# Optimization experiments

Hardware: AMD Instinct MI355X
Metric: run time of the kernel (lower is better)

The kernel has to match this reference:

```python
import jax, jax.numpy as jnp
import numpy as np

N = 100000      # nodes
E = 1600000     # edges
IN = 128        # in_channels
HID = 32        # hidden_channels
HEADS = 4
G = 256         # number of graphs in the batch
NEG_SLOPE = 0.2


def setup_inputs() -> dict:
    key = jax.random.key(0)
    ks = jax.random.split(key, 20)
    s = 0.1
    d = {
        'x': jax.random.normal(ks[0], (N, IN), jnp.float32),
        'edge_index': jax.random.randint(ks[1], (2, E), 0, N, dtype=jnp.int64),
        'batch': jnp.sort(jax.random.randint(ks[2], (N,), 0, G, dtype=jnp.int64)),
        # conv1: IN -> HID per head, HEADS heads, concat
        'W1': jax.random.normal(ks[3], (IN, HEADS * HID), jnp.float32) * s,
        'a_src1': jax.random.normal(ks[4], (HEADS, HID), jnp.float32) * s,
        'a_dst1': jax.random.normal(ks[5], (HEADS, HID), jnp.float32) * s,
        'b1': jnp.zeros((HEADS * HID,), jnp.float32),
        # conv2: HEADS*HID -> HID per head, HEADS heads, concat
        'W2': jax.random.normal(ks[6], (HEADS * HID, HEADS * HID), jnp.float32) * s,
        'a_src2': jax.random.normal(ks[7], (HEADS, HID), jnp.float32) * s,
        'a_dst2': jax.random.normal(ks[8], (HEADS, HID), jnp.float32) * s,
        'b2': jnp.zeros((HEADS * HID,), jnp.float32),
        # conv3: HEADS*HID -> HID, 1 head, no concat (mean over heads is identity)
        'W3': jax.random.normal(ks[9], (HEADS * HID, HID), jnp.float32) * s,
        'a_src3': jax.random.normal(ks[10], (1, HID), jnp.float32) * s,
        'a_dst3': jax.random.normal(ks[11], (1, HID), jnp.float32) * s,
        'b3': jnp.zeros((HID,), jnp.float32),
        # final readout
        'fc_w': jax.random.normal(ks[12], (HID, 1), jnp.float32) * s,
        'fc_b': jnp.zeros((1,), jnp.float32),
    }
    return d


def _gat_layer(x, src, dst, W, a_s, a_d, b, concat):
    """One PyG-style GATConv: edge attention logits, per-destination softmax, scatter-aggregate."""
    n = x.shape[0]
    H, C = a_s.shape
    h = (x @ W).reshape(n, H, C)                       # [N, H, C]
    asrc = (h * a_s).sum(-1)                           # [N, H]
    adst = (h * a_d).sum(-1)                           # [N, H]
    e = jax.nn.leaky_relu(asrc[src] + adst[dst], NEG_SLOPE)   # [Etot, H]
    m = jax.ops.segment_max(e, dst, num_segments=n)    # per-dst max (self-loops guarantee non-empty)
    ex = jnp.exp(e - m[dst])
    den = jax.ops.segment_sum(ex, dst, num_segments=n)
    alpha = ex / (den[dst] + 1e-16)                    # segment softmax, [Etot, H]
    out = jax.ops.segment_sum(alpha[:, :, None] * h[src], dst, num_segments=n)  # [N, H, C]
    if concat:
        return out.reshape(n, H * C) + b
    return out.mean(axis=1) + b


def reference(x, edge_index, batch, W1, a_src1, a_dst1, b1, W2, a_src2, a_dst2, b2,
              W3, a_src3, a_dst3, b3, fc_w, fc_b):
    n = x.shape[0]
    loops = jnp.arange(n, dtype=edge_index.dtype)      # GATConv adds self-loops by default
    src = jnp.concatenate([edge_index[0], loops])
    dst = jnp.concatenate([edge_index[1], loops])

    h = jax.nn.elu(_gat_layer(x, src, dst, W1, a_src1, a_dst1, b1, True))
    h = jax.nn.elu(_gat_layer(h, src, dst, W2, a_src2, a_dst2, b2, True))
    h = jax.nn.elu(_gat_layer(h, src, dst, W3, a_src3, a_dst3, b3, False))

    counts = jax.ops.segment_sum(jnp.ones((n,), h.dtype), batch, num_segments=G)
    pooled = jax.ops.segment_sum(h, batch, num_segments=G) / jnp.maximum(counts, 1.0)[:, None]
    # dropout p=0.5 is identity in eval mode
    return pooled @ fc_w + fc_b                        # [G, 1]
```

## Files before the change

kernel.cpp:

```cpp
#include <hip/hip_runtime.h>
#include <hip/hip_bf16.h>
#include <math.h>

#define NEG_SLOPE 0.2f
#define CHUNK 6144

typedef short bf16x8 __attribute__((ext_vector_type(8)));
typedef float f32x4  __attribute__((ext_vector_type(4)));

__device__ __forceinline__ float leaky(float x){ return x > 0.f ? x : NEG_SLOPE*x; }
__device__ __forceinline__ float elu(float x){ return x > 0.f ? x : expm1f(x); }

__device__ __forceinline__ ushort f2bf(float f){
  uint u = __float_as_uint(f);
  u += 0x7fffu + ((u >> 16) & 1u);
  return (ushort)(u >> 16);
}
__device__ __forceinline__ uint pk2(float lo, float hi){
  return (uint)f2bf(lo) | ((uint)f2bf(hi) << 16);
}
__device__ __forceinline__ float2 bfpair(uint v){
  return make_float2(__uint_as_float(v << 16), __uint_as_float(v & 0xffff0000u));
}

__global__ __launch_bounds__(256) void k_histA(const int* __restrict__ ei, int E,
                                               int* __restrict__ bucketCount){
  __shared__ int hist[512];
  for (int b = threadIdx.x; b < 512; b += 256) hist[b] = 0;
  __syncthreads();
  int base = blockIdx.x * 2048;
  int cnt = min(2048, E - base);
  for (int i = threadIdx.x; i < cnt; i += 256)
    atomicAdd(&hist[ei[E + base + i] >> 8], 1);
  __syncthreads();
  for (int b = threadIdx.x; b < 512; b += 256)
    if (hist[b]) atomicAdd(&bucketCount[b], hist[b]);
}

__global__ __launch_bounds__(256) void k_scanB(const int* __restrict__ bucketCount, int NB,
                        int* __restrict__ bucketBase, int* __restrict__ gcursor, int E){
  __shared__ int s[512];
  for (int b = threadIdx.x; b < 512; b += 256)
    s[b] = (b < NB) ? bucketCount[b] : 0;
  __syncthreads();
  if (threadIdx.x == 0){
    int run = 0;
    for (int b = 0; b < NB; b++){ int v = s[b]; s[b] = run; run += v; }
  }
  __syncthreads();
  for (int b = threadIdx.x; b < NB; b += 256){
    bucketBase[b] = s[b]; gcursor[b] = s[b];
  }
  if (threadIdx.x == 0) bucketBase[NB] = E;
}

__global__ __launch_bounds__(256) void k_scatA(const int* __restrict__ ei, int E, int NB,
                         int* __restrict__ gcursor, uint* __restrict__ tmp){
  __shared__ uint stageS[CHUNK];
  __shared__ uint stageD[CHUNK];
  __shared__ int hist[512], pre[512], cur[512], gbase[512];
  __shared__ int scanArr[256];
  int tid = threadIdx.x;
  int base = blockIdx.x * CHUNK;
  int cnt = min(CHUNK, E - base);
  for (int b = tid; b < 512; b += 256) hist[b] = 0;
  __syncthreads();
  for (int i = tid; i < cnt; i += 256)
    atomicAdd(&hist[ei[E + base + i] >> 8], 1);
  __syncthreads();
  int a0 = hist[2*tid], a1 = hist[2*tid+1];
  scanArr[tid] = a0 + a1;
  __syncthreads();
  for (int st = 1; st < 256; st <<= 1){
    int v = (tid >= st) ? scanArr[tid - st] : 0;
    __syncthreads();
    scanArr[tid] += v;
    __syncthreads();
  }
  int eb = tid ? scanArr[tid-1] : 0;
  pre[2*tid] = eb;        cur[2*tid] = eb;
  pre[2*tid+1] = eb + a0; cur[2*tid+1] = eb + a0;
  if (2*tid < NB && a0 > 0)   gbase[2*tid]   = atomicAdd(&gcursor[2*tid],   a0);
  if (2*tid+1 < NB && a1 > 0) gbase[2*tid+1] = atomicAdd(&gcursor[2*tid+1], a1);
  __syncthreads();
  for (int i = tid; i < cnt; i += 256){
    int s = ei[base + i];
    int d = ei[E + base + i];
    int lpos = atomicAdd(&cur[d >> 8], 1);
    stageS[lpos] = (uint)s; stageD[lpos] = (uint)d;
  }
  __syncthreads();
  for (int i = tid; i < cnt; i += 256){
    uint d = stageD[i];
    int b = d >> 8;
    tmp[gbase[b] + (i - pre[b])] = (stageS[i] << 8) | (d & 255u);
  }
}

__global__ __launch_bounds__(256) void k_csr(const uint* __restrict__ tmp,
                      const int* __restrict__ bucketBase,
                      int N, int NB, int* __restrict__ offsets, int* __restrict__ csr){
  int b = blockIdx.x;
  int nodeBase = b << 8;
  int nNodes = min(256, N - nodeBase);
  int eBeg = bucketBase[b], eEnd = bucketBase[b+1];
  __shared__ int deg[256], cur[256];
  int tid = threadIdx.x;
  deg[tid] = 0;
  __syncthreads();
  for (int e = eBeg + tid; e < eEnd; e += 256)
    atomicAdd(&deg[tmp[e] & 255u], 1);
  __syncthreads();
  cur[tid] = deg[tid];
  __syncthreads();
  for (int st = 1; st < 256; st <<= 1){
    int w = (tid >= st) ? cur[tid - st] : 0;
    __syncthreads();
    cur[tid] += w;
    __syncthreads();
  }
  int excl = tid ? cur[tid-1] : 0;
  __syncthreads();
  cur[tid] = excl;
  if (tid < nNodes) offsets[nodeBase + tid] = eBeg + excl;
  if (b == NB-1 && tid == 0) offsets[N] = eEnd;
  __syncthreads();
  for (int e = eBeg + tid; e < eEnd; e += 256){
    uint u = tmp[e];
    int lpos = atomicAdd(&cur[u & 255u], 1);
    csr[eBeg + lpos] = (int)(u >> 8);
  }
}

template<int NT>
__global__ __launch_bounds__(256) void k_wrep(const float* __restrict__ W, ushort* __restrict__ Wf){
  int idx = blockIdx.x*256 + threadIdx.x;
  if (idx >= NT*4*64) return;
  int lane = idx & 63;
  int c = (idx >> 6) & 3;
  int t = idx >> 8;
  int col = t*16 + (lane & 15);
  int k0 = c*32 + (lane >> 4)*8;
  uint4 o;
  const float* p0 = W + (size_t)k0*(NT*16) + col;
  o.x = pk2(p0[0],          p0[NT*16]);
  o.y = pk2(p0[2*NT*16],    p0[3*NT*16]);
  o.z = pk2(p0[4*NT*16],    p0[5*NT*16]);
  o.w = pk2(p0[6*NT*16],    p0[7*NT*16]);
  *(uint4*)(Wf + (size_t)idx*8) = o;
}

template<int NT, bool A_F32>
__global__ __launch_bounds__(256) void k_mgemm(const void* __restrict__ Xv,
                     const ushort* __restrict__ Wf, ushort* __restrict__ Y, int n){
  constexpr int M = NT*16;
  int lane = threadIdx.x & 63;
  int l15 = lane & 15, q = lane >> 4;
  int wgid = blockIdx.x*4 + (threadIdx.x >> 6);
  int nchunks = (n + 15) >> 4;
  int stride = gridDim.x*4;

  bf16x8 bw[NT][4];
  #pragma unroll
  for (int t = 0; t < NT; t++)
    #pragma unroll
    for (int c = 0; c < 4; c++)
      bw[t][c] = *(const bf16x8*)(Wf + (size_t)(((t<<2)+c)*64 + lane)*8);

  int chunk = wgid;
  if (chunk >= nchunks) return;

  bf16x8 aCur[4], aNext[4];
  auto loadA = [&](int ck, bf16x8* a){
    int m = ck*16 + l15;
    if (m >= n) m = n - 1;
    if (A_F32){
      const float* X = (const float*)Xv + (size_t)m*128 + q*8;
      #pragma unroll
      for (int c = 0; c < 4; c++){
        float4 u0 = *(const float4*)(X + c*32);
        float4 u1 = *(const float4*)(X + c*32 + 4);
        uint4 pkd;
        pkd.x = pk2(u0.x, u0.y); pkd.y = pk2(u0.z, u0.w);
        pkd.z = pk2(u1.x, u1.y); pkd.w = pk2(u1.z, u1.w);
        union { uint4 u; bf16x8 v; } cv; cv.u = pkd;
        a[c] = cv.v;
      }
    } else {
      const ushort* X = (const ushort*)Xv + (size_t)m*128 + q*8;
      #pragma unroll
      for (int c = 0; c < 4; c++) a[c] = *(const bf16x8*)(X + c*32);
    }
  };

  loadA(chunk, aCur);
  while (true){
    int nx = chunk + stride;
    if (nx < nchunks) loadA(nx, aNext);
    f32x4 acc[NT];
    #pragma unroll
    for (int t = 0; t < NT; t++) acc[t] = (f32x4){0.f,0.f,0.f,0.f};
    #pragma unroll
    for (int c = 0; c < 4; c++)
      #pragma unroll
      for (int t = 0; t < NT; t++)
        acc[t] = __builtin_amdgcn_mfma_f32_16x16x32_bf16(aCur[c], bw[t][c], acc[t], 0, 0, 0);
    int rowb = chunk*16 + q*4;
    #pragma unroll
    for (int t = 0; t < NT; t++)
      #pragma unroll
      for (int r = 0; r < 4; r++){
        int row = rowb + r;
        if (row < n) Y[(size_t)row*M + t*16 + l15] = f2bf(acc[t][r]);
      }
    if (nx >= nchunks) break;
    chunk = nx;
    #pragma unroll
    for (int c = 0; c < 4; c++) aCur[c] = aNext[c];
  }
}

__global__ __launch_bounds__(256) void k_attn(const ushort* __restrict__ Hb, const float* __restrict__ a_s,
                     const float* __restrict__ a_d, float* __restrict__ asrc, float* __restrict__ adst,
                     int n, int H, int M){
  int idx = blockIdx.x*256 + threadIdx.x;
  if (idx >= n*H) return;
  int node = idx / H, h = idx - node*H;
  const uint4* r4 = (const uint4*)(Hb + (size_t)node*M + h*32);
  const float* as = a_s + h*32;
  const float* ad = a_d + h*32;
  float s1 = 0.f, s2 = 0.f;
  #pragma unroll
  for (int i = 0; i < 4; i++){
    uint4 qv = r4[i];
    uint w[4] = {qv.x, qv.y, qv.z, qv.w};
    #pragma unroll
    for (int j = 0; j < 4; j++){
      float2 f = bfpair(w[j]);
      int c = i*8 + j*2;
      s1 += f.x*as[c] + f.y*as[c+1];
      s2 += f.x*ad[c] + f.y*ad[c+1];
    }
  }
  asrc[idx] = s1; adst[idx] = s2;
}

template<bool OUT_BF16>
__global__ __launch_bounds__(256) void k_agg128f(const ushort* __restrict__ Hb,
                    const float* __restrict__ asrc, const float* __restrict__ adst,
                    const int* __restrict__ offsets, const int* __restrict__ csr_src,
                    const float* __restrict__ bias, void* __restrict__ Out, int n){
  __shared__ float lwAll[4][256];
  __shared__ int   lsAll[4][64];
  int wv = threadIdx.x >> 6;
  int lane = threadIdx.x & 63;
  float* lw = lwAll[wv];
  int*   ls = lsAll[wv];
  int node = blockIdx.x*4 + wv;
  if (node >= n) return;
  const int up = lane, ch = up*2, h0 = up >> 4;
  const uint* rows = (const uint*)Hb;
  float4 adv = *(const float4*)(adst + (size_t)node*4);
  float adh = (h0==0)?adv.x:(h0==1)?adv.y:(h0==2)?adv.z:adv.w;
  float acc0 = 0.f, acc1 = 0.f, den = 0.f;
  {
    float w = __expf(leaky(asrc[(size_t)node*4 + h0] + adh));
    float2 f = bfpair(rows[(size_t)node*64 + up]);
    den += w; acc0 += w*f.x; acc1 += w*f.y;
  }
  int j0 = offsets[node], end = offsets[node+1];
  for (int base = j0; base < end; base += 64){
    int m = min(64, end - base);
    if (lane < m){
      int s = csr_src[base + lane];
      ls[lane] = s;
      float4 a = *(const float4*)(asrc + (size_t)s*4);
      float4 w4;
      w4.x = __expf(leaky(a.x + adv.x));
      w4.y = __expf(leaky(a.y + adv.y));
      w4.z = __expf(leaky(a.z + adv.z));
      w4.w = __expf(leaky(a.w + adv.w));
      *(float4*)(lw + lane*4) = w4;
    }
    int e = 0;
    for (; e + 8 <= m; e += 8){
      int s0=ls[e+0], s1=ls[e+1], s2=ls[e+2], s3=ls[e+3];
      int s4=ls[e+4], s5=ls[e+5], s6=ls[e+6], s7=ls[e+7];
      float w0=lw[(e+0)*4+h0], w1=lw[(e+1)*4+h0], w2=lw[(e+2)*4+h0], w3=lw[(e+3)*4+h0];
      float w4=lw[(e+4)*4+h0], w5=lw[(e+5)*4+h0], w6=lw[(e+6)*4+h0], w7=lw[(e+7)*4+h0];
      uint r0 = rows[(size_t)s0*64 + up];
      uint r1 = rows[(size_t)s1*64 + up];
      uint r2 = rows[(size_t)s2*64 + up];
      uint r3 = rows[(size_t)s3*64 + up];
      uint r4 = rows[(size_t)s4*64 + up];
      uint r5 = rows[(size_t)s5*64 + up];
      uint r6 = rows[(size_t)s6*64 + up];
      uint r7 = rows[(size_t)s7*64 + up];
      float2 f0=bfpair(r0), f1=bfpair(r1), f2=bfpair(r2), f3=bfpair(r3);
      float2 f4=bfpair(r4), f5=bfpair(r5), f6=bfpair(r6), f7=bfpair(r7);
      den  += ((w0+w1)+(w2+w3)) + ((w4+w5)+(w6+w7));
      acc0 += (w0*f0.x + w1*f1.x + w2*f2.x + w3*f3.x)
            + (w4*f4.x + w5*f5.x + w6*f6.x + w7*f7.x);
      acc1 += (w0*f0.y + w1*f1.y + w2*f2.y + w3*f3.y)
            + (w4*f4.y + w5*f5.y + w6*f6.y + w7*f7.y);
    }
    for (; e < m; e++){
      int s = ls[e];
      float w = lw[e*4 + h0];
      float2 f = bfpair(rows[(size_t)s*64 + up]);
      den += w; acc0 += w*f.x; acc1 += w*f.y;
    }
  }
  float inv = 1.f/(den + 1e-16f);
  float ox = elu(acc0*inv + bias[ch]);
  float oy = elu(acc1*inv + bias[ch+1]);
  if (OUT_BF16){
    ((uint*)Out)[(size_t)node*64 + up] = pk2(ox, oy);
  } else {
    *(float2*)((float*)Out + (size_t)node*128 + ch) = make_float2(ox, oy);
  }
}

__global__ __launch_bounds__(256) void k_agg32(const ushort* __restrict__ Hb,
                    const float* __restrict__ asrc, const float* __restrict__ adst,
                    const int* __restrict__ offsets, const int* __restrict__ csr_src,
                    const float* __restrict__ bias, float* __restrict__ Out, int n){
  __shared__ int   lsAll[4][4][16];
  __shared__ float lwAll[4][4][16];
  int wv = threadIdx.x >> 6;
  int lane = threadIdx.x & 63;
  int g = lane >> 4, i = lane & 15;
  int node = (blockIdx.x*4 + wv)*4 + g;
  if (node >= n) return;
  int* ls = lsAll[wv][g];
  float* lw = lwAll[wv][g];
  const uint* rows = (const uint*)Hb;
  float adn = adst[node];
  float acc0 = 0.f, acc1 = 0.f, den = 0.f;
  {
    float w = __expf(leaky(asrc[node] + adn));
    float2 f = bfpair(rows[(size_t)node*16 + i]);
    den += w; acc0 += w*f.x; acc1 += w*f.y;
  }
  int j0 = offsets[node], end = offsets[node+1];
  for (int base = j0; base < end; base += 16){
    int m = min(16, end - base);
    {
      int idx = base + i;
      bool v = idx < end;
      int s = v ? csr_src[idx] : node;
      ls[i] = s;
      lw[i] = v ? __expf(leaky(asrc[s] + adn)) : 0.f;
    }
    int mR = (m + 3) & ~3;
    for (int e = 0; e < mR; e += 4){
      int s0 = ls[e], s1 = ls[e+1], s2 = ls[e+2], s3 = ls[e+3];
      float w0 = lw[e], w1 = lw[e+1], w2 = lw[e+2], w3 = lw[e+3];
      uint r0 = rows[(size_t)s0*16 + i];
      uint r1 = rows[(size_t)s1*16 + i];
      uint r2 = rows[(size_t)s2*16 + i];
      uint r3 = rows[(size_t)s3*16 + i];
      float2 f0 = bfpair(r0), f1 = bfpair(r1), f2 = bfpair(r2), f3 = bfpair(r3);
      den  += (w0 + w1) + (w2 + w3);
      acc0 += w0*f0.x + w1*f1.x + w2*f2.x + w3*f3.x;
      acc1 += w0*f0.y + w1*f1.y + w2*f2.y + w3*f3.y;
    }
  }
  float inv = 1.f/(den + 1e-16f);
  int ch = i*2;
  float2 o;
  o.x = elu(acc0*inv + bias[ch]);
  o.y = elu(acc1*inv + bias[ch+1]);
  *(float2*)(Out + (size_t)node*32 + ch) = o;
}

__global__ __launch_bounds__(256) void k_bounds(const int* __restrict__ batch, int n, int G,
                                                int* __restrict__ gstart){
  int i = blockIdx.x*256 + threadIdx.x;
  if (i >= n) return;
  int b = batch[i];
  int bp = (i > 0) ? batch[i-1] : -1;
  for (int g = bp + 1; g <= b; g++) gstart[g] = i;
  if (i == n-1){
    for (int g = b + 1; g <= G; g++) gstart[g] = n;
  }
}

__global__ __launch_bounds__(256) void k_pool2(const float* __restrict__ H3,
                     const int* __restrict__ gstart, const float* __restrict__ fcw,
                     const float* __restrict__ fcb, float* __restrict__ out, int G){
  int g = blockIdx.x;
  int s0 = gstart[g], s1 = gstart[g+1];
  int tid = threadIdx.x;
  int c = tid & 31, r = tid >> 5;
  float sum = 0.f;
  for (int i = s0 + r; i < s1; i += 8)
    sum += H3[(size_t)i*32 + c];
  __shared__ float sh[8][32];
  sh[r][c] = sum;
  __syncthreads();
  if (tid < 32){
    float t = 0.f;
    #pragma unroll
    for (int k = 0; k < 8; k++) t += sh[k][tid];
    t *= fcw[tid];
    #pragma unroll
    for (int off = 16; off; off >>= 1) t += __shfl_down(t, off, 32);
    if (tid == 0){
      float cnt = (float)(s1 - s0); if (cnt < 1.f) cnt = 1.f;
      out[g] = t/cnt + fcb[0];
    }
  }
}

extern "C" void kernel_launch(void* const* d_in, const int* in_sizes, int n_in,
                              void* d_out, int out_size, void* d_ws, size_t ws_size,
                              hipStream_t stream){
  const float* x    = (const float*)d_in[0];
  const int*   ei   = (const int*)d_in[1];
  const int*   batch= (const int*)d_in[2];
  const float* W1   = (const float*)d_in[3];
  const float* as1  = (const float*)d_in[4];
  const float* ad1  = (const float*)d_in[5];
  const float* b1   = (const float*)d_in[6];
  const float* W2   = (const float*)d_in[7];
  const float* as2  = (const float*)d_in[8];
  const float* ad2  = (const float*)d_in[9];
  const float* b2   = (const float*)d_in[10];
  const float* W3   = (const float*)d_in[11];
  const float* as3  = (const float*)d_in[12];
  const float* ad3  = (const float*)d_in[13];
  const float* b3   = (const float*)d_in[14];
  const float* fcw  = (const float*)d_in[15];
  const float* fcb  = (const float*)d_in[16];
  float* out = (float*)d_out;

  const int N = in_sizes[0] / 128;
  const int E = in_sizes[1] / 2;
  const int G = out_size;
  const int NB = (N + 255) >> 8;

  char* p = (char*)d_ws;
  auto alloc = [&](size_t bytes) -> void* {
    void* r = (void*)p;
    p += (bytes + 255) & ~(size_t)255;
    return r;
  };
  ushort* bufH   = (ushort*)alloc((size_t)N*128*sizeof(ushort));
  ushort* aggB   = (ushort*)alloc((size_t)N*128*sizeof(ushort));
  float*  bufA32 = (float*)alloc((size_t)N*32*sizeof(float));
  float*  asrc   = (float*)alloc((size_t)N*4*sizeof(float));
  float*  adst   = (float*)alloc((size_t)N*4*sizeof(float));
  int*    offsets= (int*)alloc((size_t)(N+1)*sizeof(int));
  int*    csr    = (int*)alloc((size_t)E*sizeof(int));
  uint*   tmp    = (uint*)alloc((size_t)E*sizeof(uint));
  int*    bCount = (int*)alloc(512*sizeof(int));
  int*    bBase  = (int*)alloc(520*sizeof(int));
  int*    gcursor= (int*)alloc(512*sizeof(int));
  int*    gstart = (int*)alloc((size_t)(G+1)*sizeof(int));
  ushort* Wf1    = (ushort*)alloc(8*4*64*8*sizeof(ushort));
  ushort* Wf2    = (ushort*)alloc(8*4*64*8*sizeof(ushort));
  ushort* Wf3    = (ushort*)alloc(2*4*64*8*sizeof(ushort));

  hipMemsetAsync(bCount, 0, 512*sizeof(int), stream);

  k_wrep<8><<<8, 256, 0, stream>>>(W1, Wf1);
  k_wrep<8><<<8, 256, 0, stream>>>(W2, Wf2);
  k_wrep<2><<<2, 256, 0, stream>>>(W3, Wf3);

  k_histA<<<(E+2047)/2048, 256, 0, stream>>>(ei, E, bCount);
  k_scanB<<<1, 256, 0, stream>>>(bCount, NB, bBase, gcursor, E);
  k_scatA<<<(E+CHUNK-1)/CHUNK, 256, 0, stream>>>(ei, E, NB, gcursor, tmp);
  k_csr<<<NB, 256, 0, stream>>>(tmp, bBase, N, NB, offsets, csr);
  k_bounds<<<(N+255)/256, 256, 0, stream>>>(batch, N, G, gstart);

  const int GB = 512;
  const int NWB = (N + 3)/4;
  const int NWB32 = (N + 15)/16;
  k_mgemm<8, true ><<<GB, 256, 0, stream>>>(x, Wf1, bufH, N);
  k_attn<<<(N*4+255)/256, 256, 0, stream>>>(bufH, as1, ad1, asrc, adst, N, 4, 128);
  k_agg128f<true><<<NWB, 256, 0, stream>>>(bufH, asrc, adst, offsets, csr, b1, aggB, N);
  k_mgemm<8, false><<<GB, 256, 0, stream>>>(aggB, Wf2, bufH, N);
  k_attn<<<(N*4+255)/256, 256, 0, stream>>>(bufH, as2, ad2, asrc, adst, N, 4, 128);
  k_agg128f<true><<<NWB, 256, 0, stream>>>(bufH, asrc, adst, offsets, csr, b2, aggB, N);
  k_mgemm<2, false><<<GB, 256, 0, stream>>>(aggB, Wf3, bufH, N);
  k_attn<<<(N+255)/256, 256, 0, stream>>>(bufH, as3, ad3, asrc, adst, N, 1, 32);
  k_agg32<<<NWB32, 256, 0, stream>>>(bufH, asrc, adst, offsets, csr, b3, bufA32, N);
  k_pool2<<<G, 256, 0, stream>>>(bufA32, gstart, fcw, fcb, out, G);
}
```

Baseline: 460.0 us.

## Precompute per-edge attention weights in separate edge-parallel kernel; double-buffer gathers

Adds a destination-index array to the CSR build and a new edge-parallel kernel that computes exp(leaky(asrc[s]+adst[d])) for every edge before each aggregation. The aggregation kernels then read these weights in place of gathering asrc and evaluating exp themselves. This takes that work out of the latency-bound per-node loop. The 128-channel aggregation loop is also restructured into a software-pipelined, double-buffered 8-edge gather with padding. The cost is three extra kernel launches plus writing and rereading a 1.6M×4 float weight buffer and a cdst array.

Result: slower. 494.1 us (+7.4%).

```diff
diff --git a/kernel.cpp b/kernel.cpp
--- a/kernel.cpp
+++ b/kernel.cpp
@@ -99,7 +99,8 @@
 
 __global__ __launch_bounds__(256) void k_csr(const uint* __restrict__ tmp,
                       const int* __restrict__ bucketBase,
-                      int N, int NB, int* __restrict__ offsets, int* __restrict__ csr){
+                      int N, int NB, int* __restrict__ offsets, int* __restrict__ csr,
+                      int* __restrict__ cdst){
   int b = blockIdx.x;
   int nodeBase = b << 8;
   int nNodes = min(256, N - nodeBase);
@@ -129,6 +130,7 @@
     uint u = tmp[e];
     int lpos = atomicAdd(&cur[u & 255u], 1);
     csr[eBeg + lpos] = (int)(u >> 8);
+    cdst[eBeg + lpos] = nodeBase + (int)(u & 255u);
   }
 }
 
@@ -245,9 +247,31 @@
   asrc[idx] = s1; adst[idx] = s2;
 }
 
+template<int H>
+__global__ __launch_bounds__(256) void k_ew(const int* __restrict__ csr,
+                     const int* __restrict__ cdst, const float* __restrict__ asrc,
+                     const float* __restrict__ adst, float* __restrict__ wexp, int E){
+  int e = blockIdx.x*256 + threadIdx.x;
+  if (e >= E) return;
+  int s = csr[e], d = cdst[e];
+  if (H == 4){
+    float4 a = *(const float4*)(asrc + (size_t)s*4);
+    float4 b = *(const float4*)(adst + (size_t)d*4);
+    float4 w;
+    w.x = __expf(leaky(a.x + b.x));
+    w.y = __expf(leaky(a.y + b.y));
+    w.z = __expf(leaky(a.z + b.z));
+    w.w = __expf(leaky(a.w + b.w));
+    *(float4*)(wexp + (size_t)e*4) = w;
+  } else {
+    wexp[e] = __expf(leaky(asrc[s] + adst[d]));
+  }
+}
+
 template<bool OUT_BF16>
 __global__ __launch_bounds__(256) void k_agg128f(const ushort* __restrict__ Hb,
                     const float* __restrict__ asrc, const float* __restrict__ adst,
+                    const float* __restrict__ wexp,
                     const int* __restrict__ offsets, const int* __restrict__ csr_src,
                     const float* __restrict__ bias, void* __restrict__ Out, int n){
   __shared__ float lwAll[4][256];
@@ -260,6 +284,7 @@
   if (node >= n) return;
   const int up = lane, ch = up*2, h0 = up >> 4;
   const uint* rows = (const uint*)Hb;
+  int j0 = offsets[node], end = offsets[node+1];
   float4 adv = *(const float4*)(adst + (size_t)node*4);
   float adh = (h0==0)?adv.x:(h0==1)?adv.y:(h0==2)?adv.z:adv.w;
   float acc0 = 0.f, acc1 = 0.f, den = 0.f;
@@ -268,47 +293,40 @@
     float2 f = bfpair(rows[(size_t)node*64 + up]);
     den += w; acc0 += w*f.x; acc1 += w*f.y;
   }
-  int j0 = offsets[node], end = offsets[node+1];
   for (int base = j0; base < end; base += 64){
     int m = min(64, end - base);
-    if (lane < m){
-      int s = csr_src[base + lane];
+    int mR = (m + 7) & ~7;
+    if (lane < mR){
+      bool v = lane < m;
+      int s = v ? csr_src[base + lane] : node;
       ls[lane] = s;
-      float4 a = *(const float4*)(asrc + (size_t)s*4);
-      float4 w4;
-      w4.x = __expf(leaky(a.x + adv.x));
-      w4.y = __expf(leaky(a.y + adv.y));
-      w4.z = __expf(leaky(a.z + adv.z));
-      w4.w = __expf(leaky(a.w + adv.w));
+      float4 w4 = v ? *(const float4*)(wexp + (size_t)(base + lane)*4)
+                    : make_float4(0.f, 0.f, 0.f, 0.f);
       *(float4*)(lw + lane*4) = w4;
     }
-    int e = 0;
-    for (; e + 8 <= m; e += 8){
-      int s0=ls[e+0], s1=ls[e+1], s2=ls[e+2], s3=ls[e+3];
-      int s4=ls[e+4], s5=ls[e+5], s6=ls[e+6], s7=ls[e+7];
-      float w0=lw[(e+0)*4+h0], w1=lw[(e+1)*4+h0], w2=lw[(e+2)*4+h0], w3=lw[(e+3)*4+h0];
-      float w4=lw[(e+4)*4+h0], w5=lw[(e+5)*4+h0], w6=lw[(e+6)*4+h0], w7=lw[(e+7)*4+h0];
-      uint r0 = rows[(size_t)s0*64 + up];
-      uint r1 = rows[(size_t)s1*64 + up];
-      uint r2 = rows[(size_t)s2*64 + up];
-      uint r3 = rows[(size_t)s3*64 + up];
-      uint r4 = rows[(size_t)s4*64 + up];
-      uint r5 = rows[(size_t)s5*64 + up];
-      uint r6 = rows[(size_t)s6*64 + up];
-      uint r7 = rows[(size_t)s7*64 + up];
-      float2 f0=bfpair(r0), f1=bfpair(r1), f2=bfpair(r2), f3=bfpair(r3);
-      float2 f4=bfpair(r4), f5=bfpair(r5), f6=bfpair(r6), f7=bfpair(r7);
-      den  += ((w0+w1)+(w2+w3)) + ((w4+w5)+(w6+w7));
-      acc0 += (w0*f0.x + w1*f1.x + w2*f2.x + w3*f3.x)
-            + (w4*f4.x + w5*f5.x + w6*f6.x + w7*f7.x);
-      acc1 += (w0*f0.y + w1*f1.y + w2*f2.y + w3*f3.y)
-            + (w4*f4.y + w5*f5.y + w6*f6.y + w7*f7.y);
-    }
-    for (; e < m; e++){
-      int s = ls[e];
-      float w = lw[e*4 + h0];
-      float2 f = bfpair(rows[(size_t)s*64 + up]);
-      den += w; acc0 += w*f.x; acc1 += w*f.y;
+    int   sA[8]; float wA[8]; uint rA[8];
+    int   sB[8]; float wB[8]; uint rB[8];
+    #pragma unroll
+    for (int k = 0; k < 8; k++){ sA[k] = ls[k]; wA[k] = lw[k*4 + h0]; }
+    #pragma unroll
+    for (int k = 0; k < 8; k++) rA[k] = rows[(size_t)sA[k]*64 + up];
+    for (int e = 8; e < mR; e += 8){
+      #pragma unroll
+      for (int k = 0; k < 8; k++){ sB[k] = ls[e + k]; wB[k] = lw[(e + k)*4 + h0]; }
+      #pragma unroll
+      for (int k = 0; k < 8; k++) rB[k] = rows[(size_t)sB[k]*64 + up];
+      #pragma unroll
+      for (int k = 0; k < 8; k++){
+        float2 f = bfpair(rA[k]);
+        den += wA[k]; acc0 += wA[k]*f.x; acc1 += wA[k]*f.y;
+      }
+      #pragma unroll
+      for (int k = 0; k < 8; k++){ rA[k] = rB[k]; wA[k] = wB[k]; }
+    }
+    #pragma unroll
+    for (int k = 0; k < 8; k++){
+      float2 f = bfpair(rA[k]);
+      den += wA[k]; acc0 += wA[k]*f.x; acc1 += wA[k]*f.y;
     }
   }
   float inv = 1.f/(den + 1e-16f);
@@ -323,6 +341,7 @@
 
 __global__ __launch_bounds__(256) void k_agg32(const ushort* __restrict__ Hb,
                     const float* __restrict__ asrc, const float* __restrict__ adst,
+                    const float* __restrict__ wexp,
                     const int* __restrict__ offsets, const int* __restrict__ csr_src,
                     const float* __restrict__ bias, float* __restrict__ Out, int n){
   __shared__ int   lsAll[4][4][16];
@@ -335,6 +354,7 @@
   int* ls = lsAll[wv][g];
   float* lw = lwAll[wv][g];
   const uint* rows = (const uint*)Hb;
+  int j0 = offsets[node], end = offsets[node+1];
   float adn = adst[node];
   float acc0 = 0.f, acc1 = 0.f, den = 0.f;
   {
@@ -342,7 +362,6 @@
     float2 f = bfpair(rows[(size_t)node*16 + i]);
     den += w; acc0 += w*f.x; acc1 += w*f.y;
   }
-  int j0 = offsets[node], end = offsets[node+1];
   for (int base = j0; base < end; base += 16){
     int m = min(16, end - base);
     {
@@ -350,7 +369,7 @@
       bool v = idx < end;
       int s = v ? csr_src[idx] : node;
       ls[i] = s;
-      lw[i] = v ? __expf(leaky(asrc[s] + adn)) : 0.f;
+      lw[i] = v ? wexp[idx] : 0.f;
     }
     int mR = (m + 3) & ~3;
     for (int e = 0; e < mR; e += 4){
@@ -453,6 +472,8 @@
   float*  adst   = (float*)alloc((size_t)N*4*sizeof(float));
   int*    offsets= (int*)alloc((size_t)(N+1)*sizeof(int));
   int*    csr    = (int*)alloc((size_t)E*sizeof(int));
+  int*    cdst   = (int*)alloc((size_t)E*sizeof(int));
+  float*  wexp   = (float*)alloc((size_t)E*4*sizeof(float));
   uint*   tmp    = (uint*)alloc((size_t)E*sizeof(uint));
   int*    bCount = (int*)alloc(512*sizeof(int));
   int*    bBase  = (int*)alloc(520*sizeof(int));
@@ -471,20 +492,24 @@
   k_histA<<<(E+2047)/2048, 256, 0, stream>>>(ei, E, bCount);
   k_scanB<<<1, 256, 0, stream>>>(bCount, NB, bBase, gcursor, E);
   k_scatA<<<(E+CHUNK-1)/CHUNK, 256, 0, stream>>>(ei, E, NB, gcursor, tmp);
-  k_csr<<<NB, 256, 0, stream>>>(tmp, bBase, N, NB, offsets, csr);
+  k_csr<<<NB, 256, 0, stream>>>(tmp, bBase, N, NB, offsets, csr, cdst);
   k_bounds<<<(N+255)/256, 256, 0, stream>>>(batch, N, G, gstart);
 
   const int GB = 512;
+  const int EB = (E + 255)/256;
   const int NWB = (N + 3)/4;
   const int NWB32 = (N + 15)/16;
   k_mgemm<8, true ><<<GB, 256, 0, stream>>>(x, Wf1, bufH, N);
   k_attn<<<(N*4+255)/256, 256, 0, stream>>>(bufH, as1, ad1, asrc, adst, N, 4, 128);
-  k_agg128f<true><<<NWB, 256, 0, stream>>>(bufH, asrc, adst, offsets, csr, b1, aggB, N);
+  k_ew<4><<<EB, 256, 0, stream>>>(csr, cdst, asrc, adst, wexp, E);
+  k_agg128f<true><<<NWB, 256, 0, stream>>>(bufH, asrc, adst, wexp, offsets, csr, b1, aggB, N);
   k_mgemm<8, false><<<GB, 256, 0, stream>>>(aggB, Wf2, bufH, N);
   k_attn<<<(N*4+255)/256, 256, 0, stream>>>(bufH, as2, ad2, asrc, adst, N, 4, 128);
-  k_agg128f<true><<<NWB, 256, 0, stream>>>(bufH, asrc, adst, offsets, csr, b2, aggB, N);
+  k_ew<4><<<EB, 256, 0, stream>>>(csr, cdst, asrc, adst, wexp, E);
+  k_agg128f<true><<<NWB, 256, 0, stream>>>(bufH, asrc, adst, wexp, offsets, csr, b2, aggB, N);
   k_mgemm<2, false><<<GB, 256, 0, stream>>>(aggB, Wf3, bufH, N);
   k_attn<<<(N+255)/256, 256, 0, stream>>>(bufH, as3, ad3, asrc, adst, N, 1, 32);
-  k_agg32<<<NWB32, 256, 0, stream>>>(bufH, asrc, adst, offsets, csr, b3, bufA32, N);
+  k_ew<1><<<EB, 256, 0, stream>>>(csr, cdst, asrc, adst, wexp, E);
+  k_agg32<<<NWB32, 256, 0, stream>>>(bufH, asrc, adst, wexp, offsets, csr, b3, bufA32, N);
   k_pool2<<<G, 256, 0, stream>>>(bufA32, gstart, fcw, fcb, out, G);
 }
```

## Fold attention vectors into GEMM weights and software-pipeline edge gathers

Applied to the files above, without the earlier changes.

Precomputes W·a_src and W·a_dst as an extra 16-column MFMA tile, so each GEMM also emits the per-node attention logits and the three separate k_attn kernels are removed. This saves a full re-read of the hidden features per layer plus three launches. The logits are now computed from bf16-rounded folded weights rather than from the bf16 hidden features, which slightly changes numerics. The 128-wide aggregation kernel now broadcasts source indices with readlane instead of going through shared memory, and double-buffers groups of eight row gathers so loads overlap the accumulation.

New measurement: 448.5 us. -2.5%, faster.

```diff
diff --git a/kernel.cpp b/kernel.cpp
--- a/kernel.cpp
+++ b/kernel.cpp
@@ -132,27 +132,51 @@
   }
 }
 
-template<int NT>
-__global__ __launch_bounds__(256) void k_wrep(const float* __restrict__ W, ushort* __restrict__ Wf){
+template<int NT, int H>
+__global__ __launch_bounds__(256) void k_wrepA(const float* __restrict__ W,
+                    const float* __restrict__ a_s, const float* __restrict__ a_d,
+                    ushort* __restrict__ Wf){
+  constexpr int NTT = NT + 1;
+  constexpr int M = NT*16;
   int idx = blockIdx.x*256 + threadIdx.x;
-  if (idx >= NT*4*64) return;
+  if (idx >= NTT*4*64) return;
   int lane = idx & 63;
   int c = (idx >> 6) & 3;
   int t = idx >> 8;
-  int col = t*16 + (lane & 15);
+  int j = lane & 15;
   int k0 = c*32 + (lane >> 4)*8;
+  float vals[8];
+  if (t < NT){
+    int col = t*16 + j;
+    const float* p0 = W + (size_t)k0*M + col;
+    #pragma unroll
+    for (int r = 0; r < 8; r++) vals[r] = p0[(size_t)r*M];
+  } else {
+    #pragma unroll
+    for (int r = 0; r < 8; r++) vals[r] = 0.f;
+    if (j < 2*H){
+      int h = (j < H) ? j : (j - H);
+      const float* av = (j < H) ? (a_s + h*32) : (a_d + h*32);
+      #pragma unroll
+      for (int r = 0; r < 8; r++){
+        const float* wr = W + (size_t)(k0 + r)*M + h*32;
+        float s = 0.f;
+        for (int cc = 0; cc < 32; cc++) s += wr[cc]*av[cc];
+        vals[r] = s;
+      }
+    }
+  }
   uint4 o;
-  const float* p0 = W + (size_t)k0*(NT*16) + col;
-  o.x = pk2(p0[0],          p0[NT*16]);
-  o.y = pk2(p0[2*NT*16],    p0[3*NT*16]);
-  o.z = pk2(p0[4*NT*16],    p0[5*NT*16]);
-  o.w = pk2(p0[6*NT*16],    p0[7*NT*16]);
+  o.x = pk2(vals[0], vals[1]); o.y = pk2(vals[2], vals[3]);
+  o.z = pk2(vals[4], vals[5]); o.w = pk2(vals[6], vals[7]);
   *(uint4*)(Wf + (size_t)idx*8) = o;
 }
 
-template<int NT, bool A_F32>
+template<int NT, bool A_F32, int H>
 __global__ __launch_bounds__(256) void k_mgemm(const void* __restrict__ Xv,
-                     const ushort* __restrict__ Wf, ushort* __restrict__ Y, int n){
+                     const ushort* __restrict__ Wf, ushort* __restrict__ Y,
+                     float* __restrict__ asrc, float* __restrict__ adst, int n){
+  constexpr int NTT = NT + 1;
   constexpr int M = NT*16;
   int lane = threadIdx.x & 63;
   int l15 = lane & 15, q = lane >> 4;
@@ -160,9 +184,9 @@
   int nchunks = (n + 15) >> 4;
   int stride = gridDim.x*4;
 
-  bf16x8 bw[NT][4];
+  bf16x8 bw[NTT][4];
   #pragma unroll
-  for (int t = 0; t < NT; t++)
+  for (int t = 0; t < NTT; t++)
     #pragma unroll
     for (int c = 0; c < 4; c++)
       bw[t][c] = *(const bf16x8*)(Wf + (size_t)(((t<<2)+c)*64 + lane)*8);
@@ -197,13 +221,13 @@
   while (true){
     int nx = chunk + stride;
     if (nx < nchunks) loadA(nx, aNext);
-    f32x4 acc[NT];
-    #pragma unroll
-    for (int t = 0; t < NT; t++) acc[t] = (f32x4){0.f,0.f,0.f,0.f};
+    f32x4 acc[NTT];
+    #pragma unroll
+    for (int t = 0; t < NTT; t++) acc[t] = (f32x4){0.f,0.f,0.f,0.f};
     #pragma unroll
     for (int c = 0; c < 4; c++)
       #pragma unroll
-      for (int t = 0; t < NT; t++)
+      for (int t = 0; t < NTT; t++)
         acc[t] = __builtin_amdgcn_mfma_f32_16x16x32_bf16(aCur[c], bw[t][c], acc[t], 0, 0, 0);
     int rowb = chunk*16 + q*4;
     #pragma unroll
@@ -213,36 +237,20 @@
         int row = rowb + r;
         if (row < n) Y[(size_t)row*M + t*16 + l15] = f2bf(acc[t][r]);
       }
+    #pragma unroll
+    for (int r = 0; r < 4; r++){
+      int row = rowb + r;
+      if (row < n){
+        float v = acc[NT][r];
+        if (l15 < H)           asrc[(size_t)row*H + l15]       = v;
+        else if (l15 < 2*H)    adst[(size_t)row*H + (l15 - H)] = v;
+      }
+    }
     if (nx >= nchunks) break;
     chunk = nx;
     #pragma unroll
     for (int c = 0; c < 4; c++) aCur[c] = aNext[c];
   }
-}
-
-__global__ __launch_bounds__(256) void k_attn(const ushort* __restrict__ Hb, const float* __restrict__ a_s,
-                     const float* __restrict__ a_d, float* __restrict__ asrc, float* __restrict__ adst,
-                     int n, int H, int M){
-  int idx = blockIdx.x*256 + threadIdx.x;
-  if (idx >= n*H) return;
-  int node = idx / H, h = idx - node*H;
-  const uint4* r4 = (const uint4*)(Hb + (size_t)node*M + h*32);
-  const float* as = a_s + h*32;
-  const float* ad = a_d + h*32;
-  float s1 = 0.f, s2 = 0.f;
-  #pragma unroll
-  for (int i = 0; i < 4; i++){
-    uint4 qv = r4[i];
-    uint w[4] = {qv.x, qv.y, qv.z, qv.w};
-    #pragma unroll
-    for (int j = 0; j < 4; j++){
-      float2 f = bfpair(w[j]);
-      int c = i*8 + j*2;
-      s1 += f.x*as[c] + f.y*as[c+1];
-      s2 += f.x*ad[c] + f.y*ad[c+1];
-    }
-  }
-  asrc[idx] = s1; adst[idx] = s2;
 }
 
 template<bool OUT_BF16>
@@ -251,15 +259,14 @@
                     const int* __restrict__ offsets, const int* __restrict__ csr_src,
                     const float* __restrict__ bias, void* __restrict__ Out, int n){
   __shared__ float lwAll[4][256];
-  __shared__ int   lsAll[4][64];
   int wv = threadIdx.x >> 6;
   int lane = threadIdx.x & 63;
   float* lw = lwAll[wv];
-  int*   ls = lsAll[wv];
   int node = blockIdx.x*4 + wv;
   if (node >= n) return;
   const int up = lane, ch = up*2, h0 = up >> 4;
   const uint* rows = (const uint*)Hb;
+  int j0 = offsets[node], end = offsets[node+1];
   float4 adv = *(const float4*)(adst + (size_t)node*4);
   float adh = (h0==0)?adv.x:(h0==1)?adv.y:(h0==2)?adv.z:adv.w;
   float acc0 = 0.f, acc1 = 0.f, den = 0.f;
@@ -268,47 +275,54 @@
     float2 f = bfpair(rows[(size_t)node*64 + up]);
     den += w; acc0 += w*f.x; acc1 += w*f.y;
   }
-  int j0 = offsets[node], end = offsets[node+1];
   for (int base = j0; base < end; base += 64){
     int m = min(64, end - base);
+    int mR = (m + 7) & ~7;
+    int sreg = node;
     if (lane < m){
-      int s = csr_src[base + lane];
-      ls[lane] = s;
-      float4 a = *(const float4*)(asrc + (size_t)s*4);
+      sreg = csr_src[base + lane];
+      float4 a = *(const float4*)(asrc + (size_t)sreg*4);
       float4 w4;
       w4.x = __expf(leaky(a.x + adv.x));
       w4.y = __expf(leaky(a.y + adv.y));
       w4.z = __expf(leaky(a.z + adv.z));
       w4.w = __expf(leaky(a.w + adv.w));
       *(float4*)(lw + lane*4) = w4;
-    }
-    int e = 0;
-    for (; e + 8 <= m; e += 8){
-      int s0=ls[e+0], s1=ls[e+1], s2=ls[e+2], s3=ls[e+3];
-      int s4=ls[e+4], s5=ls[e+5], s6=ls[e+6], s7=ls[e+7];
-      float w0=lw[(e+0)*4+h0], w1=lw[(e+1)*4+h0], w2=lw[(e+2)*4+h0], w3=lw[(e+3)*4+h0];
-      float w4=lw[(e+4)*4+h0], w5=lw[(e+5)*4+h0], w6=lw[(e+6)*4+h0], w7=lw[(e+7)*4+h0];
-      uint r0 = rows[(size_t)s0*64 + up];
-      uint r1 = rows[(size_t)s1*64 + up];
-      uint r2 = rows[(size_t)s2*64 + up];
-      uint r3 = rows[(size_t)s3*64 + up];
-      uint r4 = rows[(size_t)s4*64 + up];
-      uint r5 = rows[(size_t)s5*64 + up];
-      uint r6 = rows[(size_t)s6*64 + up];
-      uint r7 = rows[(size_t)s7*64 + up];
-      float2 f0=bfpair(r0), f1=bfpair(r1), f2=bfpair(r2), f3=bfpair(r3);
-      float2 f4=bfpair(r4), f5=bfpair(r5), f6=bfpair(r6), f7=bfpair(r7);
-      den  += ((w0+w1)+(w2+w3)) + ((w4+w5)+(w6+w7));
-      acc0 += (w0*f0.x + w1*f1.x + w2*f2.x + w3*f3.x)
-            + (w4*f4.x + w5*f5.x + w6*f6.x + w7*f7.x);
-      acc1 += (w0*f0.y + w1*f1.y + w2*f2.y + w3*f3.y)
-            + (w4*f4.y + w5*f5.y + w6*f6.y + w7*f7.y);
-    }
-    for (; e < m; e++){
-      int s = ls[e];
-      float w = lw[e*4 + h0];
-      float2 f = bfpair(rows[(size_t)s*64 + up]);
-      den += w; acc0 += w*f.x; acc1 += w*f.y;
+    } else if (lane < mR){
+      *(float4*)(lw + lane*4) = make_float4(0.f, 0.f, 0.f, 0.f);
+    }
+    uint rA[8]; float wA[8];
+    uint rB[8]; float wB[8];
+    auto loadGroup = [&](int e, uint* r, float* w){
+      #pragma unroll
+      for (int k = 0; k < 8; k++){
+        int s = __builtin_amdgcn_readlane(sreg, e + k);
+        r[k] = rows[(size_t)(uint)s*64 + up];
+      }
+      #pragma unroll
+      for (int k = 0; k < 8; k++) w[k] = lw[(e + k)*4 + h0];
+    };
+    auto consume = [&](const uint* r, const float* w){
+      #pragma unroll
+      for (int k = 0; k < 8; k++){
+        float2 f = bfpair(r[k]);
+        den += w[k]; acc0 += w[k]*f.x; acc1 += w[k]*f.y;
+      }
+    };
+    loadGroup(0, rA, wA);
+    int e = 8;
+    for (; e + 16 <= mR; e += 16){
+      loadGroup(e, rB, wB);
+      consume(rA, wA);
+      loadGroup(e + 8, rA, wA);
+      consume(rB, wB);
+    }
+    if (e < mR){
+      loadGroup(e, rB, wB);
+      consume(rA, wA);
+      consume(rB, wB);
+    } else {
+      consume(rA, wA);
     }
   }
   float inv = 1.f/(den + 1e-16f);
@@ -458,15 +472,15 @@
   int*    bBase  = (int*)alloc(520*sizeof(int));
   int*    gcursor= (int*)alloc(512*sizeof(int));
   int*    gstart = (int*)alloc((size_t)(G+1)*sizeof(int));
-  ushort* Wf1    = (ushort*)alloc(8*4*64*8*sizeof(ushort));
-  ushort* Wf2    = (ushort*)alloc(8*4*64*8*sizeof(ushort));
-  ushort* Wf3    = (ushort*)alloc(2*4*64*8*sizeof(ushort));
+  ushort* Wf1    = (ushort*)alloc(9*4*64*8*sizeof(ushort));
+  ushort* Wf2    = (ushort*)alloc(9*4*64*8*sizeof(ushort));
+  ushort* Wf3    = (ushort*)alloc(3*4*64*8*sizeof(ushort));
 
   hipMemsetAsync(bCount, 0, 512*sizeof(int), stream);
 
-  k_wrep<8><<<8, 256, 0, stream>>>(W1, Wf1);
-  k_wrep<8><<<8, 256, 0, stream>>>(W2, Wf2);
-  k_wrep<2><<<2, 256, 0, stream>>>(W3, Wf3);
+  k_wrepA<8,4><<<9, 256, 0, stream>>>(W1, as1, ad1, Wf1);
+  k_wrepA<8,4><<<9, 256, 0, stream>>>(W2, as2, ad2, Wf2);
+  k_wrepA<2,1><<<3, 256, 0, stream>>>(W3, as3, ad3, Wf3);
 
   k_histA<<<(E+2047)/2048, 256, 0, stream>>>(ei, E, bCount);
   k_scanB<<<1, 256, 0, stream>>>(bCount, NB, bBase, gcursor, E);
@@ -477,14 +491,11 @@
   const int GB = 512;
   const int NWB = (N + 3)/4;
   const int NWB32 = (N + 15)/16;
-  k_mgemm<8, true ><<<GB, 256, 0, stream>>>(x, Wf1, bufH, N);
-  k_attn<<<(N*4+255)/256, 256, 0, stream>>>(bufH, as1, ad1, asrc, adst, N, 4, 128);
+  k_mgemm<8, true , 4><<<GB, 256, 0, stream>>>(x, Wf1, bufH, asrc, adst, N);
   k_agg128f<true><<<NWB, 256, 0, stream>>>(bufH, asrc, adst, offsets, csr, b1, aggB, N);
-  k_mgemm<8, false><<<GB, 256, 0, stream>>>(aggB, Wf2, bufH, N);
-  k_attn<<<(N*4+255)/256, 256, 0, stream>>>(bufH, as2, ad2, asrc, adst, N, 4, 128);
+  k_mgemm<8, false, 4><<<GB, 256, 0, stream>>>(aggB, Wf2, bufH, asrc, adst, N);
   k_agg128f<true><<<NWB, 256, 0, stream>>>(bufH, asrc, adst, offsets, csr, b2, aggB, N);
-  k_mgemm<2, false><<<GB, 256, 0, stream>>>(aggB, Wf3, bufH, N);
-  k_attn<<<(N+255)/256, 256, 0, stream>>>(bufH, as3, ad3, asrc, adst, N, 1, 32);
+  k_mgemm<2, false, 1><<<GB, 256, 0, stream>>>(aggB, Wf3, bufH, asrc, adst, N);
   k_agg32<<<NWB32, 256, 0, stream>>>(bufH, asrc, adst, offsets, csr, b3, bufA32, N);
   k_pool2<<<G, 256, 0, stream>>>(bufA32, gstart, fcw, fcb, out, G);
 }
```
